# Kernel tuning notes

Measured on AMD Instinct MI355X. Metric: run time of the kernel, lower is better.

The kernel has to match this reference:

```python
import jax, jax.numpy as jnp
import numpy as np

D_MODEL = 1024
N_HEAD = 16
HEAD_DIM = D_MODEL // N_HEAD
BATCH = 2
SEQ = 2048


def setup_inputs() -> dict:
    key = jax.random.key(0)
    ks = jax.random.split(key, 5)
    std = np.sqrt(2.0 / (D_MODEL + D_MODEL)).astype(np.float32)
    return {
        "in_features": jax.random.normal(ks[0], (BATCH, SEQ, D_MODEL), dtype=jnp.float32),
        "Wq": jax.random.normal(ks[1], (D_MODEL, D_MODEL), dtype=jnp.float32) * std,
        "Wk": jax.random.normal(ks[2], (D_MODEL, D_MODEL), dtype=jnp.float32) * std,
        "Wv": jax.random.normal(ks[3], (D_MODEL, D_MODEL), dtype=jnp.float32) * std,
        "Wo": jax.random.normal(ks[4], (D_MODEL, D_MODEL), dtype=jnp.float32) * std,
    }


def reference(in_features, Wq, Wk, Wv, Wo):
    B, S, _ = in_features.shape
    # projections: x @ W (custom Linear stores weight as [in, out], no bias)
    q = (in_features @ Wq).reshape(B, S, N_HEAD, HEAD_DIM).transpose(0, 2, 1, 3)  # [B,H,S,Dh]
    k = (in_features @ Wk).reshape(B, S, N_HEAD, HEAD_DIM).transpose(0, 2, 1, 3)
    v = (in_features @ Wv).reshape(B, S, N_HEAD, HEAD_DIM).transpose(0, 2, 1, 3)
    scale = HEAD_DIM ** (-0.5)
    scores = jnp.einsum("bhqd,bhkd->bhqk", q, k) * scale  # [B,H,S,S]
    causal = jnp.tril(jnp.ones((S, S), dtype=bool))
    scores = jnp.where(causal, scores, -jnp.inf)
    attn = jax.nn.softmax(scores, axis=-1)
    ctx = jnp.einsum("bhqk,bhkd->bhqd", attn, v)  # [B,H,S,Dh]
    ctx = ctx.transpose(0, 2, 1, 3).reshape(B, S, D_MODEL)
    return ctx @ Wo
```

## Files before the change

### kernel.cpp

```cpp
#include <hip/hip_runtime.h>
#include <hip/hip_bf16.h>

#define DM 1024
#define NH 16
#define HD 64
#define B_ 2
#define S_ 2048
#define M_ (B_*S_)

typedef __attribute__((ext_vector_type(8))) short bf16x8;
typedef __attribute__((ext_vector_type(4))) float f32x4;

__device__ __forceinline__ float bf2f(ushort u) {
  union { unsigned u32; float f; } c; c.u32 = ((unsigned)u) << 16; return c.f;
}
__device__ __forceinline__ ushort f2bf(float f) {
  union { float f; unsigned u32; } c; c.f = f;
  unsigned u = c.u32;
  unsigned r = (u + 0x7fffu + ((u >> 16) & 1u)) >> 16;
  return (ushort)r;
}
__device__ __forceinline__ unsigned fbits(float f) {
  union { float f; unsigned u; } c; c.f = f; return c.u;
}

__device__ __forceinline__ void async16(const ushort* g, ushort* l) {
  __builtin_amdgcn_global_load_lds((const __attribute__((address_space(1))) void*)g,
                                   (__attribute__((address_space(3))) void*)l, 16, 0, 0);
}

__global__ void cvt_prep(const float* __restrict__ x, const float* __restrict__ W0,
                         const float* __restrict__ W1, const float* __restrict__ W2,
                         const float* __restrict__ W3, ushort* __restrict__ wt,
                         ushort* __restrict__ xb) {
  __shared__ float tile[64][65];
  int z = blockIdx.z;
  int tx = threadIdx.x, ty = threadIdx.y;
  if (z == 4) {
    int tid = ty * 64 + tx;
    size_t base4 = ((size_t)blockIdx.y * 16 + blockIdx.x) * 4096;
    const float4* xv = (const float4*)x;
    ushort4* ov = (ushort4*)xb;
    #pragma unroll
    for (int k = 0; k < 16; ++k) {
      float4 v = xv[base4 + k * 256 + tid];
      ushort4 o;
      o.x = f2bf(v.x); o.y = f2bf(v.y); o.z = f2bf(v.z); o.w = f2bf(v.w);
      ov[base4 + k * 256 + tid] = o;
    }
    return;
  }
  const float* W = (z == 0) ? W0 : (z == 1) ? W1 : (z == 2) ? W2 : W3;
  ushort* Wt = wt + (size_t)z * (DM * DM);
  int c0 = blockIdx.x * 64, r0 = blockIdx.y * 64;
  #pragma unroll
  for (int i = ty; i < 64; i += 4) tile[i][tx] = W[(size_t)(r0 + i) * DM + c0 + tx];
  __syncthreads();
  #pragma unroll
  for (int i = ty; i < 64; i += 4) Wt[(size_t)(c0 + i) * DM + r0 + tx] = f2bf(tile[tx][i]);
}

template <int MODE>
__device__ __forceinline__ void gemm_body(const ushort* __restrict__ A,
                                          const ushort* __restrict__ Bt,
                                          ushort* __restrict__ Cb,
                                          float* __restrict__ Cf,
                                          ushort* As, ushort* Bs, ushort* Ts) {
  const int K = DM;
  int m0 = blockIdx.y * 128;
  int n0 = blockIdx.x * 128;
  int t = threadIdx.x;
  int lane = t & 63, wave = t >> 6;
  int wm = (wave >> 1) * 64, wn = (wave & 1) * 64;
  int lrow = lane & 15, quad = lane >> 4;

  int Ra = wave * 32;
  int srow = lane >> 2, scol = (lane & 3) * 8;

  f32x4 acc[4][4];
  #pragma unroll
  for (int r = 0; r < 4; ++r)
    #pragma unroll
    for (int c = 0; c < 4; ++c) acc[r][c] = (f32x4){0.f, 0.f, 0.f, 0.f};

  for (int k0 = 0; k0 < K; k0 += 32) {
    const ushort* ga = A + (size_t)(m0 + Ra + srow) * K + k0 + scol;
    const ushort* gb = Bt + (size_t)(n0 + Ra + srow) * K + k0 + scol;
    async16(ga,            As + Ra * 32);
    async16(ga + 16 * K,   As + (Ra + 16) * 32);
    async16(gb,            Bs + Ra * 32);
    async16(gb + 16 * K,   Bs + (Ra + 16) * 32);
    __syncthreads();

    bf16x8 af[4], bfr[4];
    #pragma unroll
    for (int r = 0; r < 4; ++r)
      af[r] = *(const bf16x8*)(As + (wm + r * 16 + lrow) * 32 + quad * 8);
    #pragma unroll
    for (int c = 0; c < 4; ++c)
      bfr[c] = *(const bf16x8*)(Bs + (wn + c * 16 + lrow) * 32 + quad * 8);
    #pragma unroll
    for (int r = 0; r < 4; ++r)
      #pragma unroll
      for (int c = 0; c < 4; ++c)
        acc[r][c] = __builtin_amdgcn_mfma_f32_16x16x32_bf16(af[r], bfr[c], acc[r][c], 0, 0, 0);
    __syncthreads();
  }

  if constexpr (MODE == 2) {
    int bb = m0 >> 11;
    int s0base = m0 & 2047;
    #pragma unroll
    for (int H = 0; H < 2; ++H) {
      __syncthreads();
      if ((wave >> 1) == H) {
        #pragma unroll
        for (int r = 0; r < 4; ++r)
          #pragma unroll
          for (int c = 0; c < 4; ++c) {
            uint2 pk;
            pk.x = (unsigned)f2bf(acc[r][c][0]) | ((unsigned)f2bf(acc[r][c][1]) << 16);
            pk.y = (unsigned)f2bf(acc[r][c][2]) | ((unsigned)f2bf(acc[r][c][3]) << 16);
            *(uint2*)(Ts + (wn + c * 16 + lrow) * 72 + r * 16 + quad * 4) = pk;
          }
      }
      __syncthreads();
      #pragma unroll
      for (int i = 0; i < 4; ++i) {
        int id = t + i * 256;
        int nn = id >> 3, col = (id & 7) * 8;
        uint4 v = *(const uint4*)(Ts + nn * 72 + col);
        int h2 = (n0 >> 6) + (nn >> 6), d2 = nn & 63;
        size_t dst = (((size_t)(bb * NH + h2)) * HD + d2) * (size_t)S_ + s0base + H * 64 + col;
        *(uint4*)(Cb + dst) = v;
      }
    }
  } else {
    #pragma unroll
    for (int r = 0; r < 4; ++r) {
      #pragma unroll
      for (int c = 0; c < 4; ++c) {
        #pragma unroll
        for (int e = 0; e < 4; ++e) {
          int m = m0 + wm + r * 16 + quad * 4 + e;
          int n = n0 + wn + c * 16 + lrow;
          if (MODE == 0) {
            Cf[(size_t)m * DM + n] = acc[r][c][e];
          } else {
            int b = m >> 11, s = m & 2047, h = n >> 6, d = n & 63;
            Cb[(((size_t)(b * NH + h)) * S_ + s) * HD + d] = f2bf(acc[r][c][e]);
          }
        }
      }
    }
  }
}

__global__ __launch_bounds__(256, 2) void gemm_qkv(const ushort* __restrict__ A,
                                                   const ushort* __restrict__ wt,
                                                   ushort* __restrict__ qkv) {
  __shared__ __align__(16) ushort As[128 * 32];
  __shared__ __align__(16) ushort Bs[128 * 32];
  __shared__ __align__(16) ushort Ts[128 * 72];
  int z = blockIdx.z;
  if (z < 2)
    gemm_body<1>(A, wt + (size_t)z * (DM * DM), qkv + (size_t)z * ((size_t)M_ * DM),
                 nullptr, As, Bs, Ts);
  else
    gemm_body<2>(A, wt + (size_t)2 * (DM * DM), qkv + (size_t)2 * ((size_t)M_ * DM),
                 nullptr, As, Bs, Ts);
}

__global__ __launch_bounds__(256, 2) void gemm_out(const ushort* __restrict__ A,
                                                   const ushort* __restrict__ wt,
                                                   float* __restrict__ C) {
  __shared__ __align__(16) ushort As[128 * 32];
  __shared__ __align__(16) ushort Bs[128 * 32];
  gemm_body<0>(A, wt, nullptr, C, As, Bs, nullptr);
}

#define EXPC 0.18033688011f

struct AttnState {
  f32x4 o[4];
  float l;
};

template <bool MASKED>
__device__ __forceinline__ void attn_tile_compute(
    int q0, int kt, bf16x8 qf0, bf16x8 qf1,
    const bf16x8 kf0[4], const bf16x8 kf1[4],
    const bf16x8 vf0[4], const bf16x8 vf1[4],
    ushort* pl, AttnState& st, int lrow, int quad) {
  f32x4 s[4];
  #pragma unroll
  for (int c = 0; c < 4; ++c) {
    f32x4 z = (f32x4){0.f, 0.f, 0.f, 0.f};
    z = __builtin_amdgcn_mfma_f32_16x16x32_bf16(kf0[c], qf0, z, 0, 0, 0);
    z = __builtin_amdgcn_mfma_f32_16x16x32_bf16(kf1[c], qf1, z, 0, 0, 0);
    s[c] = z;
  }
  int q = q0 + lrow;
  #pragma unroll
  for (int c = 0; c < 4; ++c) {
    float pv[4];
    #pragma unroll
    for (int e = 0; e < 4; ++e) {
      float v = __builtin_amdgcn_exp2f(s[c][e] * EXPC);
      if (MASKED) {
        int key = kt + c * 16 + quad * 4 + e;
        v = (key <= q) ? v : 0.f;
      }
      pv[e] = v;
      st.l += v;
    }
    uint2 pk;
    pk.x = __builtin_amdgcn_perm(fbits(pv[1]), fbits(pv[0]), 0x07060302u);
    pk.y = __builtin_amdgcn_perm(fbits(pv[3]), fbits(pv[2]), 0x07060302u);
    *(uint2*)(pl + lrow * 72 + c * 16 + quad * 4) = pk;
  }
  bf16x8 pf0 = *(const bf16x8*)(pl + lrow * 72 + quad * 8);
  bf16x8 pf1 = *(const bf16x8*)(pl + lrow * 72 + 32 + quad * 8);
  #pragma unroll
  for (int dt = 0; dt < 4; ++dt) {
    st.o[dt] = __builtin_amdgcn_mfma_f32_16x16x32_bf16(pf0, vf0[dt], st.o[dt], 0, 0, 0);
    st.o[dt] = __builtin_amdgcn_mfma_f32_16x16x32_bf16(pf1, vf1[dt], st.o[dt], 0, 0, 0);
  }
}

__global__ __launch_bounds__(256, 2) void attn_mfma(const ushort* __restrict__ Q,
                                                    const ushort* __restrict__ Kmat,
                                                    const ushort* __restrict__ Vt,
                                                    ushort* __restrict__ ctx) {
  __shared__ __align__(16) ushort Ks[2][64 * 72];
  __shared__ __align__(16) ushort Vs[2][64 * 72];
  __shared__ __align__(16) ushort plds[4][16 * 72];
  int t = threadIdx.x;
  int lane = t & 63, wave = t >> 6;
  int lrow = lane & 15, quad = lane >> 4;
  int bh = blockIdx.y;
  int p = blockIdx.x;
  int qt_lo = p, qt_hi = 31 - p;
  const ushort* Kb = Kmat + (size_t)bh * S_ * HD;
  const ushort* Vb = Vt + (size_t)bh * HD * S_;
  ushort* pl = plds[wave];
  int b = bh >> 4, h = bh & 15;

  int r0 = t >> 3, s0 = (t & 7) * 8;
  int r1 = (t + 256) >> 3, s1 = s0;

  int q0_lo = qt_lo * 64 + wave * 16;
  int q0_hi = qt_hi * 64 + wave * 16;
  const ushort* Qlo = Q + ((size_t)bh * S_ + q0_lo) * HD;
  const ushort* Qhi = Q + ((size_t)bh * S_ + q0_hi) * HD;
  bf16x8 qlo0 = *(const bf16x8*)(Qlo + (size_t)lrow * HD + quad * 8);
  bf16x8 qlo1 = *(const bf16x8*)(Qlo + (size_t)lrow * HD + 32 + quad * 8);
  bf16x8 qhi0 = *(const bf16x8*)(Qhi + (size_t)lrow * HD + quad * 8);
  bf16x8 qhi1 = *(const bf16x8*)(Qhi + (size_t)lrow * HD + 32 + quad * 8);

  AttnState lo, hi;
  #pragma unroll
  for (int i = 0; i < 4; ++i) {
    lo.o[i] = (f32x4){0.f, 0.f, 0.f, 0.f}; hi.o[i] = (f32x4){0.f, 0.f, 0.f, 0.f};
  }
  lo.l = 0.f; hi.l = 0.f;

  int kend = qt_hi * 64;
  int lo_end = qt_lo * 64;

  {
    uint4 ka = *(const uint4*)(Kb + (size_t)r0 * HD + s0);
    uint4 kb2 = *(const uint4*)(Kb + (size_t)r1 * HD + s1);
    uint4 va = *(const uint4*)(Vb + (size_t)r0 * S_ + s0);
    uint4 vb2 = *(const uint4*)(Vb + (size_t)r1 * S_ + s1);
    *(uint4*)(Ks[0] + r0 * 72 + s0) = ka;
    *(uint4*)(Ks[0] + r1 * 72 + s1) = kb2;
    *(uint4*)(Vs[0] + r0 * 72 + s0) = va;
    *(uint4*)(Vs[0] + r1 * 72 + s1) = vb2;
  }
  __syncthreads();

  for (int kt = 0; kt <= kend; kt += 64) {
    int cur = (kt >> 6) & 1, nxt = cur ^ 1;
    bool has_next = (kt < kend);

    uint4 ka, kb2, va, vb2;
    if (has_next) {
      int ktn = kt + 64;
      ka  = *(const uint4*)(Kb + (size_t)(ktn + r0) * HD + s0);
      kb2 = *(const uint4*)(Kb + (size_t)(ktn + r1) * HD + s1);
      va  = *(const uint4*)(Vb + (size_t)r0 * S_ + ktn + s0);
      vb2 = *(const uint4*)(Vb + (size_t)r1 * S_ + ktn + s1);
    }

    bf16x8 kf0[4], kf1[4], vf0[4], vf1[4];
    #pragma unroll
    for (int c = 0; c < 4; ++c) {
      const ushort* kr = Ks[cur] + (c * 16 + lrow) * 72;
      kf0[c] = *(const bf16x8*)(kr + quad * 8);
      kf1[c] = *(const bf16x8*)(kr + 32 + quad * 8);
      const ushort* vr = Vs[cur] + (c * 16 + lrow) * 72;
      vf0[c] = *(const bf16x8*)(vr + quad * 8);
      vf1[c] = *(const bf16x8*)(vr + 32 + quad * 8);
    }

    if (kt < kend)
      attn_tile_compute<false>(q0_hi, kt, qhi0, qhi1, kf0, kf1, vf0, vf1, pl, hi, lrow, quad);
    else
      attn_tile_compute<true>(q0_hi, kt, qhi0, qhi1, kf0, kf1, vf0, vf1, pl, hi, lrow, quad);
    if (kt < lo_end)
      attn_tile_compute<false>(q0_lo, kt, qlo0, qlo1, kf0, kf1, vf0, vf1, pl, lo, lrow, quad);
    else if (kt == lo_end)
      attn_tile_compute<true>(q0_lo, kt, qlo0, qlo1, kf0, kf1, vf0, vf1, pl, lo, lrow, quad);

    if (has_next) {
      *(uint4*)(Ks[nxt] + r0 * 72 + s0) = ka;
      *(uint4*)(Ks[nxt] + r1 * 72 + s1) = kb2;
      *(uint4*)(Vs[nxt] + r0 * 72 + s0) = va;
      *(uint4*)(Vs[nxt] + r1 * 72 + s1) = vb2;
    }
    __syncthreads();
  }

  #pragma unroll
  for (int half = 0; half < 2; ++half) {
    AttnState& st = half ? hi : lo;
    int q0 = half ? q0_hi : q0_lo;
    float l = st.l;
    l += __shfl_xor(l, 16);
    l += __shfl_xor(l, 32);
    float rl = 1.0f / l;
    #pragma unroll
    for (int e = 0; e < 4; ++e) {
      float rinv = __shfl(rl, quad * 4 + e);
      int q = q0 + quad * 4 + e;
      #pragma unroll
      for (int dt = 0; dt < 4; ++dt)
        ctx[((size_t)b * S_ + q) * DM + h * HD + dt * 16 + lrow] = f2bf(st.o[dt][e] * rinv);
    }
  }
}

extern "C" void kernel_launch(void* const* d_in, const int* in_sizes, int n_in,
                              void* d_out, int out_size, void* d_ws, size_t ws_size,
                              hipStream_t stream) {
  const float* x  = (const float*)d_in[0];
  const float* Wq = (const float*)d_in[1];
  const float* Wk = (const float*)d_in[2];
  const float* Wv = (const float*)d_in[3];
  const float* Wo = (const float*)d_in[4];
  float* out = (float*)d_out;
  ushort* ws = (ushort*)d_ws;

  ushort* xb  = ws;
  ushort* wt  = xb + (size_t)M_ * DM;
  ushort* qkv = wt + (size_t)4 * DM * DM;
  ushort* ctx = qkv + (size_t)3 * M_ * DM;

  cvt_prep<<<dim3(16, 16, 5), dim3(64, 4), 0, stream>>>(x, Wq, Wk, Wv, Wo, wt, xb);
  gemm_qkv<<<dim3(DM / 128, M_ / 128, 3), 256, 0, stream>>>(xb, wt, qkv);
  attn_mfma<<<dim3(16, B_ * NH), 256, 0, stream>>>(qkv, qkv + (size_t)M_ * DM,
                                                   qkv + (size_t)2 * M_ * DM, ctx);
  gemm_out<<<dim3(DM / 128, M_ / 128), 256, 0, stream>>>(ctx, wt + (size_t)3 * DM * DM, out);
}
```

Measured before the change: 187.4 us.

## Shrink output GEMM tile to 128x64, alias QKV smem, split attention P buffers

The output projection GEMM becomes templated on N-tile width and runs with 64-column tiles, doubling its grid from 256 to 512 blocks so the GPU's compute units are better filled. The QKV GEMM aliases its transpose staging buffer onto the A/B tile shared memory to cut LDS footprint. The attention kernel gives the hi and lo query halves separate P staging buffers, removing a write-after-read hazard on the shared buffer and letting the two tile computations overlap. The cost is lower per-block data reuse in the output GEMM and more LDS in attention.

```diff
diff --git a/kernel.cpp b/kernel.cpp
--- a/kernel.cpp
+++ b/kernel.cpp
@@ -60,49 +60,51 @@
   for (int i = ty; i < 64; i += 4) Wt[(size_t)(c0 + i) * DM + r0 + tx] = f2bf(tile[tx][i]);
 }
 
-template <int MODE>
+template <int MODE, int BN>
 __device__ __forceinline__ void gemm_body(const ushort* __restrict__ A,
                                           const ushort* __restrict__ Bt,
                                           ushort* __restrict__ Cb,
                                           float* __restrict__ Cf,
                                           ushort* As, ushort* Bs, ushort* Ts) {
   const int K = DM;
+  constexpr int CN = BN / 32;
   int m0 = blockIdx.y * 128;
-  int n0 = blockIdx.x * 128;
+  int n0 = blockIdx.x * BN;
   int t = threadIdx.x;
   int lane = t & 63, wave = t >> 6;
-  int wm = (wave >> 1) * 64, wn = (wave & 1) * 64;
+  int wm = (wave >> 1) * 64, wn = (wave & 1) * (BN / 2);
   int lrow = lane & 15, quad = lane >> 4;
 
   int Ra = wave * 32;
+  int Rb = wave * (BN / 4);
   int srow = lane >> 2, scol = (lane & 3) * 8;
 
-  f32x4 acc[4][4];
+  f32x4 acc[4][CN];
   #pragma unroll
   for (int r = 0; r < 4; ++r)
     #pragma unroll
-    for (int c = 0; c < 4; ++c) acc[r][c] = (f32x4){0.f, 0.f, 0.f, 0.f};
+    for (int c = 0; c < CN; ++c) acc[r][c] = (f32x4){0.f, 0.f, 0.f, 0.f};
 
   for (int k0 = 0; k0 < K; k0 += 32) {
     const ushort* ga = A + (size_t)(m0 + Ra + srow) * K + k0 + scol;
-    const ushort* gb = Bt + (size_t)(n0 + Ra + srow) * K + k0 + scol;
-    async16(ga,            As + Ra * 32);
-    async16(ga + 16 * K,   As + (Ra + 16) * 32);
-    async16(gb,            Bs + Ra * 32);
-    async16(gb + 16 * K,   Bs + (Ra + 16) * 32);
+    const ushort* gb = Bt + (size_t)(n0 + Rb + srow) * K + k0 + scol;
+    async16(ga,          As + Ra * 32);
+    async16(ga + 16 * K, As + (Ra + 16) * 32);
+    async16(gb,          Bs + Rb * 32);
+    if (BN == 128) async16(gb + 16 * K, Bs + (Rb + 16) * 32);
     __syncthreads();
 
-    bf16x8 af[4], bfr[4];
+    bf16x8 af[4], bfr[CN];
     #pragma unroll
     for (int r = 0; r < 4; ++r)
       af[r] = *(const bf16x8*)(As + (wm + r * 16 + lrow) * 32 + quad * 8);
     #pragma unroll
-    for (int c = 0; c < 4; ++c)
+    for (int c = 0; c < CN; ++c)
       bfr[c] = *(const bf16x8*)(Bs + (wn + c * 16 + lrow) * 32 + quad * 8);
     #pragma unroll
     for (int r = 0; r < 4; ++r)
       #pragma unroll
-      for (int c = 0; c < 4; ++c)
+      for (int c = 0; c < CN; ++c)
         acc[r][c] = __builtin_amdgcn_mfma_f32_16x16x32_bf16(af[r], bfr[c], acc[r][c], 0, 0, 0);
     __syncthreads();
   }
@@ -139,7 +141,7 @@
     #pragma unroll
     for (int r = 0; r < 4; ++r) {
       #pragma unroll
-      for (int c = 0; c < 4; ++c) {
+      for (int c = 0; c < CN; ++c) {
         #pragma unroll
         for (int e = 0; e < 4; ++e) {
           int m = m0 + wm + r * 16 + quad * 4 + e;
@@ -159,24 +161,25 @@
 __global__ __launch_bounds__(256, 2) void gemm_qkv(const ushort* __restrict__ A,
                                                    const ushort* __restrict__ wt,
                                                    ushort* __restrict__ qkv) {
-  __shared__ __align__(16) ushort As[128 * 32];
-  __shared__ __align__(16) ushort Bs[128 * 32];
-  __shared__ __align__(16) ushort Ts[128 * 72];
+  __shared__ __align__(16) ushort smem[9216];
+  ushort* As = smem;
+  ushort* Bs = smem + 4096;
+  ushort* Ts = smem;
   int z = blockIdx.z;
   if (z < 2)
-    gemm_body<1>(A, wt + (size_t)z * (DM * DM), qkv + (size_t)z * ((size_t)M_ * DM),
-                 nullptr, As, Bs, Ts);
+    gemm_body<1, 128>(A, wt + (size_t)z * (DM * DM), qkv + (size_t)z * ((size_t)M_ * DM),
+                      nullptr, As, Bs, Ts);
   else
-    gemm_body<2>(A, wt + (size_t)2 * (DM * DM), qkv + (size_t)2 * ((size_t)M_ * DM),
-                 nullptr, As, Bs, Ts);
+    gemm_body<2, 128>(A, wt + (size_t)2 * (DM * DM), qkv + (size_t)2 * ((size_t)M_ * DM),
+                      nullptr, As, Bs, Ts);
 }
 
 __global__ __launch_bounds__(256, 2) void gemm_out(const ushort* __restrict__ A,
                                                    const ushort* __restrict__ wt,
                                                    float* __restrict__ C) {
   __shared__ __align__(16) ushort As[128 * 32];
-  __shared__ __align__(16) ushort Bs[128 * 32];
-  gemm_body<0>(A, wt, nullptr, C, As, Bs, nullptr);
+  __shared__ __align__(16) ushort Bs[64 * 32];
+  gemm_body<0, 64>(A, wt, nullptr, C, As, Bs, nullptr);
 }
 
 #define EXPC 0.18033688011f
@@ -234,7 +237,7 @@
                                                     ushort* __restrict__ ctx) {
   __shared__ __align__(16) ushort Ks[2][64 * 72];
   __shared__ __align__(16) ushort Vs[2][64 * 72];
-  __shared__ __align__(16) ushort plds[4][16 * 72];
+  __shared__ __align__(16) ushort plds[8][16 * 72];
   int t = threadIdx.x;
   int lane = t & 63, wave = t >> 6;
   int lrow = lane & 15, quad = lane >> 4;
@@ -243,7 +246,8 @@
   int qt_lo = p, qt_hi = 31 - p;
   const ushort* Kb = Kmat + (size_t)bh * S_ * HD;
   const ushort* Vb = Vt + (size_t)bh * HD * S_;
-  ushort* pl = plds[wave];
+  ushort* pl_hi = plds[wave];
+  ushort* pl_lo = plds[wave + 4];
   int b = bh >> 4, h = bh & 15;
 
   int r0 = t >> 3, s0 = (t & 7) * 8;
@@ -305,13 +309,13 @@
     }
 
     if (kt < kend)
-      attn_tile_compute<false>(q0_hi, kt, qhi0, qhi1, kf0, kf1, vf0, vf1, pl, hi, lrow, quad);
+      attn_tile_compute<false>(q0_hi, kt, qhi0, qhi1, kf0, kf1, vf0, vf1, pl_hi, hi, lrow, quad);
     else
-      attn_tile_compute<true>(q0_hi, kt, qhi0, qhi1, kf0, kf1, vf0, vf1, pl, hi, lrow, quad);
+      attn_tile_compute<true>(q0_hi, kt, qhi0, qhi1, kf0, kf1, vf0, vf1, pl_hi, hi, lrow, quad);
     if (kt < lo_end)
-      attn_tile_compute<false>(q0_lo, kt, qlo0, qlo1, kf0, kf1, vf0, vf1, pl, lo, lrow, quad);
+      attn_tile_compute<false>(q0_lo, kt, qlo0, qlo1, kf0, kf1, vf0, vf1, pl_lo, lo, lrow, quad);
     else if (kt == lo_end)
-      attn_tile_compute<true>(q0_lo, kt, qlo0, qlo1, kf0, kf1, vf0, vf1, pl, lo, lrow, quad);
+      attn_tile_compute<true>(q0_lo, kt, qlo0, qlo1, kf0, kf1, vf0, vf1, pl_lo, lo, lrow, quad);
 
     if (has_next) {
       *(uint4*)(Ks[nxt] + r0 * 72 + s0) = ka;
@@ -361,5 +365,5 @@
   gemm_qkv<<<dim3(DM / 128, M_ / 128, 3), 256, 0, stream>>>(xb, wt, qkv);
   attn_mfma<<<dim3(16, B_ * NH), 256, 0, stream>>>(qkv, qkv + (size_t)M_ * DM,
                                                    qkv + (size_t)2 * M_ * DM, ctx);
-  gemm_out<<<dim3(DM / 128, M_ / 128), 256, 0, stream>>>(ctx, wt + (size_t)3 * DM * DM, out);
-}
+  gemm_out<<<dim3(DM / 64, M_ / 128), 256, 0, stream>>>(ctx, wt + (size_t)3 * DM * DM, out);
+}
```

New measurement: 183.2 us. -2.3%, faster.
